# Optimization experiments

Measured on AMD Instinct MI355X. Metric: run time of the kernel, lower is better.

## Reference

```python
import jax, jax.numpy as jnp
import numpy as np

D_K = 64  # module-level constant in source
NEG = -1e9


def setup_inputs() -> dict:
    key = jax.random.key(0)
    k1, k2, k3, k4 = jax.random.split(key, 4)
    B, H, S, D = 4, 16, 2048, 64
    query = jax.random.normal(k1, (B, H, S, D), dtype=jnp.float32)
    key_t = jax.random.normal(k2, (B, H, S, D), dtype=jnp.float32)
    value = jax.random.normal(k3, (B, H, S, D), dtype=jnp.float32)
    mask = jax.random.randint(k4, (B, 1, S, S), 0, 2) == 1  # bool, broadcast over heads
    return {"query": query, "key": key_t, "value": value, "mask": mask}


def reference(query, key, value, mask):
    # scores = QK^T / sqrt(d_k)   [B,H,S,S]
    scores = jnp.einsum("bhqd,bhkd->bhqk", query, key) / jnp.sqrt(jnp.float32(D_K))
    # masked_fill_(mask, -1e9)
    scores = jnp.where(mask, jnp.float32(NEG), scores)
    # non-standard: multiply masked scores by V, then log_softmax over last dim
    out = jnp.einsum("bhqk,bhkd->bhqd", scores, value)  # [B,H,S,d_v]
    return jax.nn.log_softmax(out, axis=-1)
```

## Files before the change

kernel.cpp:

```cpp
#include <hip/hip_runtime.h>
#include <hip/hip_bf16.h>


typedef __attribute__((ext_vector_type(8))) short bf16x8;
typedef __attribute__((ext_vector_type(16))) float f32x16;

#define NEGV (-1e9f)

__device__ inline unsigned cvt_bf16(float f) {
    unsigned u = __builtin_bit_cast(unsigned, f);
    u += 0x7FFFu + ((u >> 16) & 1u);
    return u >> 16;
}
__device__ inline unsigned pk_bf16(float a, float b) {
    return cvt_bf16(a) | (cvt_bf16(b) << 16);
}
__device__ inline unsigned pk_trunc(float a, float b) {
    return __builtin_amdgcn_perm(__builtin_bit_cast(unsigned, b),
                                 __builtin_bit_cast(unsigned, a), 0x07060302u);
}

#define WS_BIT_OFF  0u
#define WS_K_OFF    2097152u
#define WS_V_OFF    18874368u
#define WS_NEED     35651584ull

__global__ __launch_bounds__(256)
void preconv(const int* __restrict__ M, const float* __restrict__ K,
             const float* __restrict__ V, unsigned long long* __restrict__ bitT,
             unsigned short* __restrict__ Kswz, unsigned short* __restrict__ Vtswz) {
    const int tid  = threadIdx.x;
    const int lane = tid & 63;
    const int wave = tid >> 6;
    const int bid  = blockIdx.x;

    if (bid < 2048) {
        const int gw = (bid * 256 + tid) >> 6;
        const int b  = gw >> 11;
        const int qt = (gw >> 8) & 7;
        const int q  = gw & 255;
        const size_t mbase = (size_t)gw * 2048;
        unsigned long long* dst = bitT + (size_t)(b * 8 + qt) * 32 * 256 + q;
#pragma unroll 4
        for (int ki = 0; ki < 32; ki++) {
            const int m = M[mbase + ki * 64 + lane];
            const unsigned long long bal = __ballot(m != 0);
            if (lane == 0) dst[ki * 256] = bal;
        }
    } else if (bid < 6144) {
        const unsigned g   = (unsigned)(bid - 2048) * 256 + tid;
        const int b4  = g & 7;
        const int row = (g >> 3) & 63;
        const int d0  = (b4 ^ (row & 7)) * 8;
        const float* src = K + (size_t)(g >> 3) * 64 + d0;
        const float4 f0 = *(const float4*)(src);
        const float4 f1 = *(const float4*)(src + 4);
        uint4 p;
        p.x = pk_trunc(f0.x, f0.y); p.y = pk_trunc(f0.z, f0.w);
        p.z = pk_trunc(f1.x, f1.y); p.w = pk_trunc(f1.z, f1.w);
        *(uint4*)&Kswz[(size_t)g * 8] = p;
    } else {
        const int j    = (bid - 6144) * 4 + wave;
        const int kgrp = j & 7;
        const int ki   = (j >> 3) & 31;
        const int bh   = j >> 8;
        const size_t vbase = ((size_t)(bh * 2048 + ki * 64 + kgrp * 8)) * 64 + lane;
        float v[8];
#pragma unroll
        for (int jj = 0; jj < 8; jj++) v[jj] = V[vbase + jj * 64];
        uint4 p;
        p.x = pk_trunc(v[0], v[1]); p.y = pk_trunc(v[2], v[3]);
        p.z = pk_trunc(v[4], v[5]); p.w = pk_trunc(v[6], v[7]);
        const size_t chunk = ((size_t)(bh * 32 + ki) * 64 + lane) * 8 + (kgrp ^ (lane & 7));
        *(uint4*)&Vtswz[chunk * 8] = p;
    }
}

__global__ __launch_bounds__(256, 4)
void attn_fast(const float* __restrict__ Q,
               const unsigned short* __restrict__ Kswz,
               const unsigned short* __restrict__ Vtswz,
               const unsigned long long* __restrict__ bitT,
               float* __restrict__ Out) {
    __shared__ __attribute__((aligned(16))) unsigned short sK[2][64 * 64];
    __shared__ __attribute__((aligned(16))) unsigned short sVt[2][64 * 64];

    const int tid  = threadIdx.x;
    const int wave = tid >> 6;
    const int lane = tid & 63;
    const int half = lane >> 5;
    const int l32  = lane & 31;

    const int bid = blockIdx.x;
    const int h   = bid & 15;
    const int qt2 = (bid >> 4) & 15;
    const int b   = bid >> 8;
    const int bh  = b * 16 + h;
    const int q0  = qt2 * 128;
    const int qt  = qt2 >> 1;
    const int qh  = qt2 & 1;

    const float* Qb = Q + (size_t)(bh * 2048 + q0) * 64;
    const unsigned short* Kt = Kswz  + ((size_t)bh << 17);
    const unsigned short* Vt = Vtswz + ((size_t)bh << 17);
    const unsigned long long* Bt = bitT + (size_t)(b * 8 + qt) * 32 * 256
                                 + qh * 128 + wave * 32 + l32;

    #define STAGE(buf, ki) do {                                                   \
        const unsigned short* kg_ = Kt + ((ki) << 12) + wave * 1024 + lane * 8;   \
        const unsigned short* vg_ = Vt + ((ki) << 12) + wave * 1024 + lane * 8;   \
        unsigned short* ks_ = &sK[buf][wave * 1024];                              \
        unsigned short* vs_ = &sVt[buf][wave * 1024];                             \
        __builtin_amdgcn_global_load_lds(                                         \
            (const __attribute__((address_space(1))) void*)kg_,                   \
            (__attribute__((address_space(3))) void*)ks_, 16, 0, 0);              \
        __builtin_amdgcn_global_load_lds(                                         \
            (const __attribute__((address_space(1))) void*)(kg_ + 512),           \
            (__attribute__((address_space(3))) void*)(ks_ + 512), 16, 0, 0);      \
        __builtin_amdgcn_global_load_lds(                                         \
            (const __attribute__((address_space(1))) void*)vg_,                   \
            (__attribute__((address_space(3))) void*)vs_, 16, 0, 0);              \
        __builtin_amdgcn_global_load_lds(                                         \
            (const __attribute__((address_space(1))) void*)(vg_ + 512),           \
            (__attribute__((address_space(3))) void*)(vs_ + 512), 16, 0, 0);      \
    } while (0)

    STAGE(0, 0);
    unsigned long long mw = Bt[0];

    bf16x8 qF[4];
    {
        const float* qr = Qb + (size_t)(wave * 32 + l32) * 64 + half * 8;
#pragma unroll
        for (int dk = 0; dk < 4; dk++) {
            const float4 f0 = *(const float4*)(qr + dk * 16);
            const float4 f1 = *(const float4*)(qr + dk * 16 + 4);
            union { bf16x8 v; unsigned u[4]; } t;
            t.u[0] = pk_bf16(f0.x * 0.125f, f0.y * 0.125f);
            t.u[1] = pk_bf16(f0.z * 0.125f, f0.w * 0.125f);
            t.u[2] = pk_bf16(f1.x * 0.125f, f1.y * 0.125f);
            t.u[3] = pk_bf16(f1.z * 0.125f, f1.w * 0.125f);
            qF[dk] = t.v;
        }
    }

    f32x16 Oacc[2];
#pragma unroll
    for (int db = 0; db < 2; db++)
#pragma unroll
        for (int r = 0; r < 16; r++) Oacc[db][r] = 0.f;

    __syncthreads();

    const int swz = (l32 & 7) << 4;

    for (int ki = 0; ki < 32; ki++) {
        const int cur = ki & 1;

        unsigned long long mwN = 0;
        if (ki < 31) {
            STAGE(cur ^ 1, ki + 1);
            mwN = Bt[(ki + 1) * 256];
        }

        const char* sKc = (const char*)sK[cur];
        const char* sVc = (const char*)sVt[cur];

#pragma unroll
        for (int jk = 0; jk < 2; jk++) {
            bf16x8 aK[4];
#pragma unroll
            for (int dk = 0; dk < 4; dk++)
                aK[dk] = *(const bf16x8*)(sKc +
                    ((((jk * 32 + l32) * 128) + dk * 32 + half * 16) ^ swz));
            bf16x8 bV[2][2];
#pragma unroll
            for (int p = 0; p < 2; p++)
#pragma unroll
                for (int db = 0; db < 2; db++)
                    bV[p][db] = *(const bf16x8*)(sVc +
                        ((((db * 32 + l32) * 128) + (jk * 2 + p) * 32 + half * 16) ^ swz));

            const unsigned b32 = (unsigned)(mw >> (jk * 32));
            const unsigned bsh = b32 >> (half * 4);

            f32x16 acc;
#pragma unroll
            for (int rg = 0; rg < 4; rg++) {
                const unsigned nib = bsh >> (rg * 8);
                acc[rg * 4 + 0] = (nib & 1u) ? NEGV : 0.f;
                acc[rg * 4 + 1] = (nib & 2u) ? NEGV : 0.f;
                acc[rg * 4 + 2] = (nib & 4u) ? NEGV : 0.f;
                acc[rg * 4 + 3] = (nib & 8u) ? NEGV : 0.f;
            }
#pragma unroll
            for (int dk = 0; dk < 4; dk++)
                acc = __builtin_amdgcn_mfma_f32_32x32x16_bf16(aK[dk], qF[dk], acc, 0, 0, 0);

#pragma unroll
            for (int p = 0; p < 2; p++) {
                const unsigned P0 = pk_trunc(acc[p * 8 + 0], acc[p * 8 + 1]);
                const unsigned P1 = pk_trunc(acc[p * 8 + 2], acc[p * 8 + 3]);
                const unsigned P2 = pk_trunc(acc[p * 8 + 4], acc[p * 8 + 5]);
                const unsigned P3 = pk_trunc(acc[p * 8 + 6], acc[p * 8 + 7]);
                auto r02 = __builtin_amdgcn_permlane32_swap(P0, P2, false, false);
                auto r13 = __builtin_amdgcn_permlane32_swap(P1, P3, false, false);
                union { bf16x8 v; unsigned u[4]; } aS;
                aS.u[0] = (unsigned)r02[0];
                aS.u[1] = (unsigned)r13[0];
                aS.u[2] = (unsigned)r02[1];
                aS.u[3] = (unsigned)r13[1];
#pragma unroll
                for (int db = 0; db < 2; db++)
                    Oacc[db] = __builtin_amdgcn_mfma_f32_32x32x16_bf16(aS.v, bV[p][db], Oacc[db], 0, 0, 0);
            }
        }

        mw = mwN;
        __syncthreads();
    }

    float* Ob = Out + (size_t)bh * 2048 * 64;
#pragma unroll
    for (int r = 0; r < 16; r++) {
        const float v0 = Oacc[0][r], v1 = Oacc[1][r];
        float mx = fmaxf(v0, v1);
#pragma unroll
        for (int off = 1; off < 32; off <<= 1)
            mx = fmaxf(mx, __shfl_xor(mx, off, 64));
        float s = __expf(v0 - mx) + __expf(v1 - mx);
#pragma unroll
        for (int off = 1; off < 32; off <<= 1)
            s += __shfl_xor(s, off, 64);
        const float lse = mx + __logf(s);
        const int qrow = q0 + wave * 32 + (r & 3) + 8 * (r >> 2) + 4 * half;
        Ob[(size_t)qrow * 64 + l32]      = v0 - lse;
        Ob[(size_t)qrow * 64 + 32 + l32] = v1 - lse;
    }
    #undef STAGE
}

__global__ __launch_bounds__(256)
void mask_pack(const int* __restrict__ M, unsigned long long* __restrict__ bitT) {
    const int lane = threadIdx.x & 63;
    const int gw   = (blockIdx.x * 256 + threadIdx.x) >> 6;
    const int b    = gw >> 11;
    const int qt   = (gw >> 8) & 7;
    const int q    = gw & 255;
    const size_t mbase = (size_t)gw * 2048;
    unsigned long long* dst = bitT + (size_t)(b * 8 + qt) * 32 * 256 + q;
#pragma unroll 4
    for (int ki = 0; ki < 32; ki++) {
        const int m = M[mbase + ki * 64 + lane];
        const unsigned long long bal = __ballot(m != 0);
        if (lane == 0) dst[ki * 256] = bal;
    }
}

__global__ __launch_bounds__(256, 4)
void attn_v10(const float* __restrict__ Q, const float* __restrict__ K,
              const float* __restrict__ V,
              const unsigned long long* __restrict__ bitT,
              float* __restrict__ Out) {
    __shared__ __attribute__((aligned(16))) unsigned short sK[2][64 * 72];
    __shared__ __attribute__((aligned(16))) unsigned short sVt[2][64 * 72];

    const int tid  = threadIdx.x;
    const int wave = tid >> 6;
    const int lane = tid & 63;
    const int half = lane >> 5;
    const int l32  = lane & 31;

    const int bid = blockIdx.x;
    const int h   = bid & 15;
    const int qt2 = (bid >> 4) & 15;
    const int b   = bid >> 8;
    const int bh  = b * 16 + h;
    const int q0  = qt2 * 128;
    const int qt  = qt2 >> 1;
    const int qh  = qt2 & 1;

    const float* Qb = Q + (size_t)(bh * 2048 + q0) * 64;
    const float* Kb = K + (size_t)bh * 2048 * 64;
    const float* Vb = V + (size_t)bh * 2048 * 64;
    const unsigned long long* Bt = bitT + (size_t)(b * 8 + qt) * 32 * 256
                                 + qh * 128 + wave * 32 + l32;

    float4 kp[4];
    float  vp[16];
    unsigned long long mw = Bt[0];
    const int krow = tid >> 4, kc4 = tid & 15;
#pragma unroll
    for (int i = 0; i < 4; i++)
        kp[i] = *(const float4*)(Kb + (size_t)(krow + i * 16) * 64 + kc4 * 4);
#pragma unroll
    for (int i = 0; i < 2; i++) {
        const int kb = (wave * 2 + i) * 8;
#pragma unroll
        for (int j = 0; j < 8; j++)
            vp[i * 8 + j] = Vb[(size_t)(kb + j) * 64 + lane];
    }

    bf16x8 qF[4];
    {
        const float* qr = Qb + (size_t)(wave * 32 + l32) * 64 + half * 8;
#pragma unroll
        for (int dk = 0; dk < 4; dk++) {
            const float4 f0 = *(const float4*)(qr + dk * 16);
            const float4 f1 = *(const float4*)(qr + dk * 16 + 4);
            union { bf16x8 v; unsigned u[4]; } t;
            t.u[0] = pk_bf16(f0.x * 0.125f, f0.y * 0.125f);
            t.u[1] = pk_bf16(f0.z * 0.125f, f0.w * 0.125f);
            t.u[2] = pk_bf16(f1.x * 0.125f, f1.y * 0.125f);
            t.u[3] = pk_bf16(f1.z * 0.125f, f1.w * 0.125f);
            qF[dk] = t.v;
        }
    }

    f32x16 Oacc[2];
#pragma unroll
    for (int db = 0; db < 2; db++)
#pragma unroll
        for (int r = 0; r < 16; r++) Oacc[db][r] = 0.f;

    for (int ki = 0; ki < 32; ki++) {
        const int cur = ki & 1;
#pragma unroll
        for (int i = 0; i < 4; i++) {
            uint2 p;
            p.x = pk_trunc(kp[i].x, kp[i].y);
            p.y = pk_trunc(kp[i].z, kp[i].w);
            *(uint2*)&sK[cur][(krow + i * 16) * 72 + kc4 * 4] = p;
        }
#pragma unroll
        for (int i = 0; i < 2; i++) {
            const int kb = (wave * 2 + i) * 8;
            uint4 p4;
            p4.x = pk_trunc(vp[i * 8 + 0], vp[i * 8 + 1]);
            p4.y = pk_trunc(vp[i * 8 + 2], vp[i * 8 + 3]);
            p4.z = pk_trunc(vp[i * 8 + 4], vp[i * 8 + 5]);
            p4.w = pk_trunc(vp[i * 8 + 6], vp[i * 8 + 7]);
            *(uint4*)&sVt[cur][lane * 72 + kb] = p4;
        }

        __syncthreads();

        unsigned long long mwN = 0;
        if (ki < 31) {
            const int kn = (ki + 1) * 64;
            mwN = Bt[(ki + 1) * 256];
#pragma unroll
            for (int i = 0; i < 4; i++)
                kp[i] = *(const float4*)(Kb + (size_t)(kn + krow + i * 16) * 64 + kc4 * 4);
#pragma unroll
            for (int i = 0; i < 2; i++) {
                const int kb = (wave * 2 + i) * 8;
#pragma unroll
                for (int j = 0; j < 8; j++)
                    vp[i * 8 + j] = Vb[(size_t)(kn + kb + j) * 64 + lane];
            }
        }

#pragma unroll
        for (int jk = 0; jk < 2; jk++) {
            bf16x8 aK[4];
#pragma unroll
            for (int dk = 0; dk < 4; dk++)
                aK[dk] = *(const bf16x8*)&sK[cur][(jk * 32 + l32) * 72 + dk * 16 + half * 8];
            bf16x8 bV[2][2];
#pragma unroll
            for (int p = 0; p < 2; p++)
#pragma unroll
                for (int db = 0; db < 2; db++)
                    bV[p][db] = *(const bf16x8*)&sVt[cur][(db * 32 + l32) * 72 + (jk * 2 + p) * 16 + half * 8];

            const unsigned b32 = (unsigned)(mw >> (jk * 32));
            const unsigned bsh = b32 >> (half * 4);

            f32x16 acc;
#pragma unroll
            for (int rg = 0; rg < 4; rg++) {
                const unsigned nib = bsh >> (rg * 8);
                acc[rg * 4 + 0] = (nib & 1u) ? NEGV : 0.f;
                acc[rg * 4 + 1] = (nib & 2u) ? NEGV : 0.f;
                acc[rg * 4 + 2] = (nib & 4u) ? NEGV : 0.f;
                acc[rg * 4 + 3] = (nib & 8u) ? NEGV : 0.f;
            }
#pragma unroll
            for (int dk = 0; dk < 4; dk++)
                acc = __builtin_amdgcn_mfma_f32_32x32x16_bf16(aK[dk], qF[dk], acc, 0, 0, 0);

#pragma unroll
            for (int p = 0; p < 2; p++) {
                const unsigned P0 = pk_trunc(acc[p * 8 + 0], acc[p * 8 + 1]);
                const unsigned P1 = pk_trunc(acc[p * 8 + 2], acc[p * 8 + 3]);
                const unsigned P2 = pk_trunc(acc[p * 8 + 4], acc[p * 8 + 5]);
                const unsigned P3 = pk_trunc(acc[p * 8 + 6], acc[p * 8 + 7]);
                auto r02 = __builtin_amdgcn_permlane32_swap(P0, P2, false, false);
                auto r13 = __builtin_amdgcn_permlane32_swap(P1, P3, false, false);
                union { bf16x8 v; unsigned u[4]; } aS;
                aS.u[0] = (unsigned)r02[0];
                aS.u[1] = (unsigned)r13[0];
                aS.u[2] = (unsigned)r02[1];
                aS.u[3] = (unsigned)r13[1];
#pragma unroll
                for (int db = 0; db < 2; db++)
                    Oacc[db] = __builtin_amdgcn_mfma_f32_32x32x16_bf16(aS.v, bV[p][db], Oacc[db], 0, 0, 0);
            }
        }

        mw = mwN;
    }

    float* Ob = Out + (size_t)bh * 2048 * 64;
#pragma unroll
    for (int r = 0; r < 16; r++) {
        const float v0 = Oacc[0][r], v1 = Oacc[1][r];
        float mx = fmaxf(v0, v1);
#pragma unroll
        for (int off = 1; off < 32; off <<= 1)
            mx = fmaxf(mx, __shfl_xor(mx, off, 64));
        float s = __expf(v0 - mx) + __expf(v1 - mx);
#pragma unroll
        for (int off = 1; off < 32; off <<= 1)
            s += __shfl_xor(s, off, 64);
        const float lse = mx + __logf(s);
        const int qrow = q0 + wave * 32 + (r & 3) + 8 * (r >> 2) + 4 * half;
        Ob[(size_t)qrow * 64 + l32]      = v0 - lse;
        Ob[(size_t)qrow * 64 + 32 + l32] = v1 - lse;
    }
}

extern "C" void kernel_launch(void* const* d_in, const int* in_sizes, int n_in,
                              void* d_out, int out_size, void* d_ws, size_t ws_size,
                              hipStream_t stream) {
    const float* Q = (const float*)d_in[0];
    const float* K = (const float*)d_in[1];
    const float* V = (const float*)d_in[2];
    const int*   M = (const int*)d_in[3];
    float* Out = (float*)d_out;
    unsigned long long* bitT = (unsigned long long*)d_ws;

    if (ws_size >= WS_NEED) {
        unsigned short* Kswz  = (unsigned short*)((char*)d_ws + WS_K_OFF);
        unsigned short* Vtswz = (unsigned short*)((char*)d_ws + WS_V_OFF);
        preconv<<<dim3(10240), dim3(256), 0, stream>>>(M, K, V, bitT, Kswz, Vtswz);
        attn_fast<<<dim3(1024), dim3(256), 0, stream>>>(Q, Kswz, Vtswz, bitT, Out);
    } else {
        mask_pack<<<dim3(2048), dim3(256), 0, stream>>>(M, bitT);
        attn_v10<<<dim3(1024), dim3(256), 0, stream>>>(Q, K, V, bitT, Out);
    }
}
```

Measured before the change: 265.9 us.

## Replace XOR-swizzled K/V tiles with padded interleaved K/V tile layout

The preconversion kernel now writes K and transposed V into one combined per-tile workspace buffer. Each row is padded to 72 bf16 elements instead of using an XOR swizzle, and the attention kernel stages a whole tile with one set of global_load_lds calls into a single padded LDS array. This removes the swizzle address arithmetic and aims to avoid LDS bank conflicts through padding instead. The mask-to-accumulator initialisation also switches from selects to a sign-extend-and-AND bit trick. In exchange, LDS use per block and the workspace requirement both grow, and part of each tile is staged with narrower 4-byte loads.

```diff
diff --git a/kernel.cpp b/kernel.cpp
--- a/kernel.cpp
+++ b/kernel.cpp
@@ -6,6 +6,7 @@
 typedef __attribute__((ext_vector_type(16))) float f32x16;
 
 #define NEGV (-1e9f)
+#define NEGBITS 0xCE6E6B28u
 
 __device__ inline unsigned cvt_bf16(float f) {
     unsigned u = __builtin_bit_cast(unsigned, f);
@@ -20,18 +21,15 @@
                                  __builtin_bit_cast(unsigned, a), 0x07060302u);
 }
 
-#define WS_BIT_OFF  0u
-#define WS_K_OFF    2097152u
-#define WS_V_OFF    18874368u
-#define WS_NEED     35651584ull
+#define WS_KV_OFF  2097152u
+#define WS_NEED    39845888ull
 
 __global__ __launch_bounds__(256)
 void preconv(const int* __restrict__ M, const float* __restrict__ K,
              const float* __restrict__ V, unsigned long long* __restrict__ bitT,
-             unsigned short* __restrict__ Kswz, unsigned short* __restrict__ Vtswz) {
+             unsigned short* __restrict__ KV) {
     const int tid  = threadIdx.x;
     const int lane = tid & 63;
-    const int wave = tid >> 6;
     const int bid  = blockIdx.x;
 
     if (bid < 2048) {
@@ -49,41 +47,40 @@
         }
     } else if (bid < 6144) {
         const unsigned g   = (unsigned)(bid - 2048) * 256 + tid;
-        const int b4  = g & 7;
-        const int row = (g >> 3) & 63;
-        const int d0  = (b4 ^ (row & 7)) * 8;
-        const float* src = K + (size_t)(g >> 3) * 64 + d0;
+        const int c        = g & 7;
+        const unsigned rid = g >> 3;
+        const int r        = rid & 63;
+        const unsigned tile = rid >> 6;
+        const float* src = K + (size_t)rid * 64 + c * 8;
         const float4 f0 = *(const float4*)(src);
         const float4 f1 = *(const float4*)(src + 4);
         uint4 p;
         p.x = pk_trunc(f0.x, f0.y); p.y = pk_trunc(f0.z, f0.w);
         p.z = pk_trunc(f1.x, f1.y); p.w = pk_trunc(f1.z, f1.w);
-        *(uint4*)&Kswz[(size_t)g * 8] = p;
+        *(uint4*)&KV[(size_t)tile * 9216 + r * 72 + c * 8] = p;
     } else {
-        const int j    = (bid - 6144) * 4 + wave;
-        const int kgrp = j & 7;
-        const int ki   = (j >> 3) & 31;
-        const int bh   = j >> 8;
-        const size_t vbase = ((size_t)(bh * 2048 + ki * 64 + kgrp * 8)) * 64 + lane;
+        const unsigned g = (unsigned)(bid - 6144) * 256 + tid;
+        const int d  = g & 63;
+        const int c  = (g >> 6) & 7;
+        const int ki = (g >> 9) & 31;
+        const int bh = g >> 14;
+        const float* src = V + ((size_t)(bh * 2048 + ki * 64 + c * 8) * 64 + d);
         float v[8];
 #pragma unroll
-        for (int jj = 0; jj < 8; jj++) v[jj] = V[vbase + jj * 64];
+        for (int j = 0; j < 8; j++) v[j] = src[j * 64];
         uint4 p;
         p.x = pk_trunc(v[0], v[1]); p.y = pk_trunc(v[2], v[3]);
         p.z = pk_trunc(v[4], v[5]); p.w = pk_trunc(v[6], v[7]);
-        const size_t chunk = ((size_t)(bh * 32 + ki) * 64 + lane) * 8 + (kgrp ^ (lane & 7));
-        *(uint4*)&Vtswz[chunk * 8] = p;
+        *(uint4*)&KV[(size_t)(bh * 32 + ki) * 9216 + 4608 + d * 72 + c * 8] = p;
     }
 }
 
 __global__ __launch_bounds__(256, 4)
 void attn_fast(const float* __restrict__ Q,
-               const unsigned short* __restrict__ Kswz,
-               const unsigned short* __restrict__ Vtswz,
+               const unsigned short* __restrict__ KV,
                const unsigned long long* __restrict__ bitT,
                float* __restrict__ Out) {
-    __shared__ __attribute__((aligned(16))) unsigned short sK[2][64 * 64];
-    __shared__ __attribute__((aligned(16))) unsigned short sVt[2][64 * 64];
+    __shared__ __attribute__((aligned(16))) unsigned short sT[2][9216];
 
     const int tid  = threadIdx.x;
     const int wave = tid >> 6;
@@ -101,28 +98,27 @@
     const int qh  = qt2 & 1;
 
     const float* Qb = Q + (size_t)(bh * 2048 + q0) * 64;
-    const unsigned short* Kt = Kswz  + ((size_t)bh << 17);
-    const unsigned short* Vt = Vtswz + ((size_t)bh << 17);
+    const unsigned short* Tg = KV + (size_t)bh * 32 * 9216;
     const unsigned long long* Bt = bitT + (size_t)(b * 8 + qt) * 32 * 256
                                  + qh * 128 + wave * 32 + l32;
 
     #define STAGE(buf, ki) do {                                                   \
-        const unsigned short* kg_ = Kt + ((ki) << 12) + wave * 1024 + lane * 8;   \
-        const unsigned short* vg_ = Vt + ((ki) << 12) + wave * 1024 + lane * 8;   \
-        unsigned short* ks_ = &sK[buf][wave * 1024];                              \
-        unsigned short* vs_ = &sVt[buf][wave * 1024];                             \
-        __builtin_amdgcn_global_load_lds(                                         \
-            (const __attribute__((address_space(1))) void*)kg_,                   \
-            (__attribute__((address_space(3))) void*)ks_, 16, 0, 0);              \
-        __builtin_amdgcn_global_load_lds(                                         \
-            (const __attribute__((address_space(1))) void*)(kg_ + 512),           \
-            (__attribute__((address_space(3))) void*)(ks_ + 512), 16, 0, 0);      \
-        __builtin_amdgcn_global_load_lds(                                         \
-            (const __attribute__((address_space(1))) void*)vg_,                   \
-            (__attribute__((address_space(3))) void*)vs_, 16, 0, 0);              \
-        __builtin_amdgcn_global_load_lds(                                         \
-            (const __attribute__((address_space(1))) void*)(vg_ + 512),           \
-            (__attribute__((address_space(3))) void*)(vs_ + 512), 16, 0, 0);      \
+        const unsigned short* g_ = Tg + (size_t)(ki) * 9216;                      \
+        unsigned short* l_ = sT[buf];                                             \
+        _Pragma("unroll")                                                         \
+        for (int q_ = 0; q_ < 4; q_++)                                            \
+            __builtin_amdgcn_global_load_lds(                                     \
+                (const __attribute__((address_space(1))) void*)                   \
+                    (g_ + q_ * 2048 + wave * 512 + lane * 8),                     \
+                (__attribute__((address_space(3))) void*)                         \
+                    (l_ + q_ * 2048 + wave * 512), 16, 0, 0);                     \
+        _Pragma("unroll")                                                         \
+        for (int s_ = 0; s_ < 2; s_++)                                            \
+            __builtin_amdgcn_global_load_lds(                                     \
+                (const __attribute__((address_space(1))) void*)                   \
+                    (g_ + 8192 + s_ * 512 + wave * 128 + lane * 2),               \
+                (__attribute__((address_space(3))) void*)                         \
+                    (l_ + 8192 + s_ * 512 + wave * 128), 4, 0, 0);                \
     } while (0)
 
     STAGE(0, 0);
@@ -152,8 +148,6 @@
 
     __syncthreads();
 
-    const int swz = (l32 & 7) << 4;
-
     for (int ki = 0; ki < 32; ki++) {
         const int cur = ki & 1;
 
@@ -163,23 +157,19 @@
             mwN = Bt[(ki + 1) * 256];
         }
 
-        const char* sKc = (const char*)sK[cur];
-        const char* sVc = (const char*)sVt[cur];
-
 #pragma unroll
         for (int jk = 0; jk < 2; jk++) {
             bf16x8 aK[4];
 #pragma unroll
             for (int dk = 0; dk < 4; dk++)
-                aK[dk] = *(const bf16x8*)(sKc +
-                    ((((jk * 32 + l32) * 128) + dk * 32 + half * 16) ^ swz));
+                aK[dk] = *(const bf16x8*)&sT[cur][(jk * 32 + l32) * 72 + dk * 16 + half * 8];
             bf16x8 bV[2][2];
 #pragma unroll
             for (int p = 0; p < 2; p++)
 #pragma unroll
                 for (int db = 0; db < 2; db++)
-                    bV[p][db] = *(const bf16x8*)(sVc +
-                        ((((db * 32 + l32) * 128) + (jk * 2 + p) * 32 + half * 16) ^ swz));
+                    bV[p][db] = *(const bf16x8*)&sT[cur][4608 + (db * 32 + l32) * 72
+                                                         + (jk * 2 + p) * 16 + half * 8];
 
             const unsigned b32 = (unsigned)(mw >> (jk * 32));
             const unsigned bsh = b32 >> (half * 4);
@@ -187,11 +177,12 @@
             f32x16 acc;
 #pragma unroll
             for (int rg = 0; rg < 4; rg++) {
-                const unsigned nib = bsh >> (rg * 8);
-                acc[rg * 4 + 0] = (nib & 1u) ? NEGV : 0.f;
-                acc[rg * 4 + 1] = (nib & 2u) ? NEGV : 0.f;
-                acc[rg * 4 + 2] = (nib & 4u) ? NEGV : 0.f;
-                acc[rg * 4 + 3] = (nib & 8u) ? NEGV : 0.f;
+#pragma unroll
+                for (int w = 0; w < 4; w++) {
+                    const int pos = rg * 8 + w;
+                    const int sb = ((int)(bsh << (31 - pos))) >> 31;
+                    acc[rg * 4 + w] = __builtin_bit_cast(float, (unsigned)sb & NEGBITS);
+                }
             }
 #pragma unroll
             for (int dk = 0; dk < 4; dk++)
@@ -442,10 +433,9 @@
     unsigned long long* bitT = (unsigned long long*)d_ws;
 
     if (ws_size >= WS_NEED) {
-        unsigned short* Kswz  = (unsigned short*)((char*)d_ws + WS_K_OFF);
-        unsigned short* Vtswz = (unsigned short*)((char*)d_ws + WS_V_OFF);
-        preconv<<<dim3(10240), dim3(256), 0, stream>>>(M, K, V, bitT, Kswz, Vtswz);
-        attn_fast<<<dim3(1024), dim3(256), 0, stream>>>(Q, Kswz, Vtswz, bitT, Out);
+        unsigned short* KV = (unsigned short*)((char*)d_ws + WS_KV_OFF);
+        preconv<<<dim3(10240), dim3(256), 0, stream>>>(M, K, V, bitT, KV);
+        attn_fast<<<dim3(1024), dim3(256), 0, stream>>>(Q, KV, bitT, Out);
     } else {
         mask_pack<<<dim3(2048), dim3(256), 0, stream>>>(M, bitT);
         attn_v10<<<dim3(1024), dim3(256), 0, stream>>>(Q, K, V, bitT, Out);
```

After: 276.6 us. 1.04x slower.
